# Kernel tuning notes

Hardware: AMD Instinct MI355X
Metric: run time of the kernel (lower is better)

## Reference

```python
import jax, jax.numpy as jnp
import numpy as np

SCALE = 100.0
ACTIVE_EPS = 1e-6


def setup_inputs() -> dict:
    key = jax.random.key(0)
    kq, kk, kv = jax.random.split(key, 3)
    B, K, D = 64, 1024, 512
    return {
        "query": jax.random.normal(kq, (B, D), dtype=jnp.float32),
        "keys": jax.random.normal(kk, (K, D), dtype=jnp.float32),
        "values": jax.random.normal(kv, (K, D), dtype=jnp.float32),
    }


def _scores(query, keys):
    # Fused, batched version of the per-key PureFFN score layers.
    # Layer k has W_up = diag(S * key[k] * d^-0.5) on active dims (|key|>1e-6),
    # b_gate = 1 on active dims, W_down[0] = 1/S on active dims. The extra
    # hidden unit (row `dim`) has zero W_down weight and never contributes.
    # PureFFN: out = W_down @ (h * sigmoid(h + b_gate)), h = W_up @ x.
    D = query.shape[-1]
    scale = D ** -0.5
    active = (jnp.abs(keys) > ACTIVE_EPS).astype(query.dtype)      # [K, D]
    u = (SCALE * scale) * query[:, None, :] * keys[None, :, :]     # [B, K, D]
    g = u * jax.nn.sigmoid(u + active[None, :, :])                 # silu with b_gate=1 on active dims
    return (1.0 / SCALE) * jnp.einsum('bkd,kd->bk', g, active)    # [B, K]


def reference(query, keys, values):
    scores = _scores(query, keys)            # [B, K]
    winner_idx = jnp.argmax(scores, axis=-1)  # [B] int
    out_values = values[winner_idx]           # [B, D] winner-take-all gather
    return out_values, winner_idx
```

## Files before the change

kernel.cpp:

```cpp
#include <hip/hip_runtime.h>
#include <stdint.h>

#define NB 64
#define NK 1024
#define ND 512
#define CHUNKS 16
#define KEYS_PER_BLOCK (NK / CHUNKS)
#define WAVES_PER_BLOCK 4
#define KEYS_PER_WAVE (KEYS_PER_BLOCK / WAVES_PER_BLOCK)

#if __has_builtin(__builtin_amdgcn_exp2f)
#define EXP2F(x) __builtin_amdgcn_exp2f(x)
#else
#define EXP2F(x) exp2f(x)
#endif
#if __has_builtin(__builtin_amdgcn_rcpf)
#define RCPF(x) __builtin_amdgcn_rcpf(x)
#else
#define RCPF(x) (1.0f / (x))
#endif

__device__ __forceinline__ float silu_term(float qc, float kv, float acc) {
    float kz = (fabsf(kv) > 1e-6f) ? kv : 0.0f;
    float u = qc * kz;
    const float NL2E = -1.4426950408889634f;
    float y = fmaf(u, NL2E, NL2E);
    float e = EXP2F(y);
    float r = RCPF(1.0f + e);
    return fmaf(u, r, acc);
}

__device__ __forceinline__ unsigned long long pack_win(float s, int k) {
    uint32_t bits = __float_as_uint(s);
    uint32_t so = (bits & 0x80000000u) ? ~bits : (bits | 0x80000000u);
    return ((unsigned long long)so << 32) | (unsigned long long)(~(uint32_t)k);
}

__global__ __launch_bounds__(256) void sia_scores(const float* __restrict__ q,
                                                  const float* __restrict__ keys,
                                                  unsigned long long* __restrict__ ws) {
    const int bidx = blockIdx.x;
    const int b = bidx >> 4;
    const int chunk = bidx & (CHUNKS - 1);
    const int tid = threadIdx.x;
    const int wave = tid >> 6;
    const int lane = tid & 63;

    const float C = 100.0f * 0.04419417382415922f;

    const float4* q4 = reinterpret_cast<const float4*>(q + b * ND + lane * 8);
    float4 qa = q4[0];
    float4 qb = q4[1];
    qa.x *= C; qa.y *= C; qa.z *= C; qa.w *= C;
    qb.x *= C; qb.y *= C; qb.z *= C; qb.w *= C;

    const int k0 = chunk * KEYS_PER_BLOCK + wave * KEYS_PER_WAVE;

    float acc[KEYS_PER_WAVE];
    #pragma unroll
    for (int i = 0; i < KEYS_PER_WAVE; ++i) {
        const float4* k4 = reinterpret_cast<const float4*>(keys + (k0 + i) * ND + lane * 8);
        float4 ka = k4[0];
        float4 kb = k4[1];
        float p = 0.0f;
        p = silu_term(qa.x, ka.x, p);
        p = silu_term(qa.y, ka.y, p);
        p = silu_term(qa.z, ka.z, p);
        p = silu_term(qa.w, ka.w, p);
        p = silu_term(qb.x, kb.x, p);
        p = silu_term(qb.y, kb.y, p);
        p = silu_term(qb.z, kb.z, p);
        p = silu_term(qb.w, kb.w, p);
        acc[i] = p;
    }

    #pragma unroll
    for (int off = 32; off > 0; off >>= 1) {
        #pragma unroll
        for (int i = 0; i < KEYS_PER_WAVE; ++i)
            acc[i] += __shfl_xor(acc[i], off, 64);
    }

    float best_s = acc[0];
    int best_j = 0;
    #pragma unroll
    for (int i = 1; i < KEYS_PER_WAVE; ++i)
        if (acc[i] > best_s) { best_s = acc[i]; best_j = i; }

    if (lane == 0)
        ws[b * 64 + chunk * WAVES_PER_BLOCK + wave] = pack_win(best_s, k0 + best_j);
}

__global__ __launch_bounds__(64) void sia_final(const unsigned long long* __restrict__ ws,
                                                const float* __restrict__ values,
                                                float* __restrict__ out) {
    const int b = blockIdx.x;
    const int lane = threadIdx.x;

    unsigned long long p = ws[b * 64 + lane];
    #pragma unroll
    for (int off = 32; off > 0; off >>= 1) {
        unsigned long long o = __shfl_xor(p, off, 64);
        if (o > p) p = o;
    }
    const uint32_t k = ~(uint32_t)(p & 0xFFFFFFFFull);

    const float4* v4 = reinterpret_cast<const float4*>(values + (size_t)k * ND) + lane * 2;
    float4* o4 = reinterpret_cast<float4*>(out + b * ND) + lane * 2;
    o4[0] = v4[0];
    o4[1] = v4[1];

    if (lane == 0)
        out[NB * ND + b] = (float)k;
}

extern "C" void kernel_launch(void* const* d_in, const int* in_sizes, int n_in,
                              void* d_out, int out_size, void* d_ws, size_t ws_size,
                              hipStream_t stream) {
    const float* q      = (const float*)d_in[0];
    const float* keys   = (const float*)d_in[1];
    const float* values = (const float*)d_in[2];
    float* out = (float*)d_out;
    unsigned long long* ws = (unsigned long long*)d_ws;

    sia_scores<<<dim3(NB * CHUNKS), dim3(256), 0, stream>>>(q, keys, ws);
    sia_final<<<dim3(NB), dim3(64), 0, stream>>>(ws, values, out);
}
```

Baseline: 19.31 us.

## Process four query rows per block to reuse key loads and hoist masking

Each block now handles four batch rows and a smaller key chunk (64 chunks of 16 keys). Every loaded key vector and its activity mask is reused across the four queries, which cuts global key traffic and repeated mask work. Per-wave winners are reduced in shared memory so each block writes one packed winner per row. The grid size stays the same, but each thread keeps more accumulators and query registers, and the block gains a shared-memory reduction and a __syncthreads.

After: 17.92 us. -7.2%, faster.

```diff
diff --git a/kernel.cpp b/kernel.cpp
--- a/kernel.cpp
+++ b/kernel.cpp
@@ -4,7 +4,8 @@
 #define NB 64
 #define NK 1024
 #define ND 512
-#define CHUNKS 16
+#define ROWS 4
+#define CHUNKS 64
 #define KEYS_PER_BLOCK (NK / CHUNKS)
 #define WAVES_PER_BLOCK 4
 #define KEYS_PER_WAVE (KEYS_PER_BLOCK / WAVES_PER_BLOCK)
@@ -20,8 +21,7 @@
 #define RCPF(x) (1.0f / (x))
 #endif
 
-__device__ __forceinline__ float silu_term(float qc, float kv, float acc) {
-    float kz = (fabsf(kv) > 1e-6f) ? kv : 0.0f;
+__device__ __forceinline__ float silu_acc(float qc, float kz, float acc) {
     float u = qc * kz;
     const float NL2E = -1.4426950408889634f;
     float y = fmaf(u, NL2E, NL2E);
@@ -36,11 +36,15 @@
     return ((unsigned long long)so << 32) | (unsigned long long)(~(uint32_t)k);
 }
 
+__device__ __forceinline__ float msk(float kv) {
+    return (fabsf(kv) > 1e-6f) ? kv : 0.0f;
+}
+
 __global__ __launch_bounds__(256) void sia_scores(const float* __restrict__ q,
                                                   const float* __restrict__ keys,
                                                   unsigned long long* __restrict__ ws) {
     const int bidx = blockIdx.x;
-    const int b = bidx >> 4;
+    const int bg = bidx >> 6;
     const int chunk = bidx & (CHUNKS - 1);
     const int tid = threadIdx.x;
     const int wave = tid >> 6;
@@ -48,47 +52,77 @@
 
     const float C = 100.0f * 0.04419417382415922f;
 
-    const float4* q4 = reinterpret_cast<const float4*>(q + b * ND + lane * 8);
-    float4 qa = q4[0];
-    float4 qb = q4[1];
-    qa.x *= C; qa.y *= C; qa.z *= C; qa.w *= C;
-    qb.x *= C; qb.y *= C; qb.z *= C; qb.w *= C;
+    float4 qa[ROWS], qb[ROWS];
+    #pragma unroll
+    for (int r = 0; r < ROWS; ++r) {
+        const float4* q4 = reinterpret_cast<const float4*>(q + (bg * ROWS + r) * ND + lane * 8);
+        qa[r] = q4[0]; qb[r] = q4[1];
+        qa[r].x *= C; qa[r].y *= C; qa[r].z *= C; qa[r].w *= C;
+        qb[r].x *= C; qb[r].y *= C; qb[r].z *= C; qb[r].w *= C;
+    }
 
     const int k0 = chunk * KEYS_PER_BLOCK + wave * KEYS_PER_WAVE;
 
-    float acc[KEYS_PER_WAVE];
+    float acc[ROWS][KEYS_PER_WAVE];
+    #pragma unroll
+    for (int r = 0; r < ROWS; ++r)
+        #pragma unroll
+        for (int i = 0; i < KEYS_PER_WAVE; ++i)
+            acc[r][i] = 0.0f;
+
     #pragma unroll
     for (int i = 0; i < KEYS_PER_WAVE; ++i) {
         const float4* k4 = reinterpret_cast<const float4*>(keys + (k0 + i) * ND + lane * 8);
         float4 ka = k4[0];
         float4 kb = k4[1];
-        float p = 0.0f;
-        p = silu_term(qa.x, ka.x, p);
-        p = silu_term(qa.y, ka.y, p);
-        p = silu_term(qa.z, ka.z, p);
-        p = silu_term(qa.w, ka.w, p);
-        p = silu_term(qb.x, kb.x, p);
-        p = silu_term(qb.y, kb.y, p);
-        p = silu_term(qb.z, kb.z, p);
-        p = silu_term(qb.w, kb.w, p);
-        acc[i] = p;
+        ka.x = msk(ka.x); ka.y = msk(ka.y); ka.z = msk(ka.z); ka.w = msk(ka.w);
+        kb.x = msk(kb.x); kb.y = msk(kb.y); kb.z = msk(kb.z); kb.w = msk(kb.w);
+        #pragma unroll
+        for (int r = 0; r < ROWS; ++r) {
+            float p = acc[r][i];
+            p = silu_acc(qa[r].x, ka.x, p);
+            p = silu_acc(qa[r].y, ka.y, p);
+            p = silu_acc(qa[r].z, ka.z, p);
+            p = silu_acc(qa[r].w, ka.w, p);
+            p = silu_acc(qb[r].x, kb.x, p);
+            p = silu_acc(qb[r].y, kb.y, p);
+            p = silu_acc(qb[r].z, kb.z, p);
+            p = silu_acc(qb[r].w, kb.w, p);
+            acc[r][i] = p;
+        }
     }
 
     #pragma unroll
     for (int off = 32; off > 0; off >>= 1) {
         #pragma unroll
-        for (int i = 0; i < KEYS_PER_WAVE; ++i)
-            acc[i] += __shfl_xor(acc[i], off, 64);
+        for (int r = 0; r < ROWS; ++r)
+            #pragma unroll
+            for (int i = 0; i < KEYS_PER_WAVE; ++i)
+                acc[r][i] += __shfl_xor(acc[r][i], off, 64);
     }
 
-    float best_s = acc[0];
-    int best_j = 0;
-    #pragma unroll
-    for (int i = 1; i < KEYS_PER_WAVE; ++i)
-        if (acc[i] > best_s) { best_s = acc[i]; best_j = i; }
+    __shared__ unsigned long long win[WAVES_PER_BLOCK][ROWS];
+    if (lane == 0) {
+        #pragma unroll
+        for (int r = 0; r < ROWS; ++r) {
+            float best_s = acc[r][0];
+            int best_j = 0;
+            #pragma unroll
+            for (int i = 1; i < KEYS_PER_WAVE; ++i)
+                if (acc[r][i] > best_s) { best_s = acc[r][i]; best_j = i; }
+            win[wave][r] = pack_win(best_s, k0 + best_j);
+        }
+    }
+    __syncthreads();
 
-    if (lane == 0)
-        ws[b * 64 + chunk * WAVES_PER_BLOCK + wave] = pack_win(best_s, k0 + best_j);
+    if (tid < ROWS) {
+        const int r = tid;
+        unsigned long long p = win[0][r];
+        #pragma unroll
+        for (int w = 1; w < WAVES_PER_BLOCK; ++w)
+            if (win[w][r] > p) p = win[w][r];
+        ws[(bg * ROWS + r) * CHUNKS + chunk] = p;
+    }
 }
 
 __global__ __launch_bounds__(64) void sia_final(const unsigned long long* __restrict__ ws,
@@ -97,7 +131,7 @@
     const int b = blockIdx.x;
     const int lane = threadIdx.x;
 
-    unsigned long long p = ws[b * 64 + lane];
+    unsigned long long p = ws[b * CHUNKS + lane];
     #pragma unroll
     for (int off = 32; off > 0; off >>= 1) {
         unsigned long long o = __shfl_xor(p, off, 64);
@@ -123,6 +157,6 @@
     float* out = (float*)d_out;
     unsigned long long* ws = (unsigned long long*)d_ws;
 
-    sia_scores<<<dim3(NB * CHUNKS), dim3(256), 0, stream>>>(q, keys, ws);
+    sia_scores<<<dim3((NB / ROWS) * CHUNKS), dim3(256), 0, stream>>>(q, keys, ws);
     sia_final<<<dim3(NB), dim3(64), 0, stream>>>(ws, values, out);
 }
```

## Stage masked key chunks in LDS and share them across four query rows

Applied to the files above, without the earlier changes.

Each block now loads a 16-key chunk of keys into shared memory once and applies the activity mask during staging. Four waves then reuse that chunk for four different query rows. Before, each block handled one query row and read its keys straight from global memory. This cuts redundant global and L2 key traffic and removes the per-element mask from the inner loop, at the cost of 32 KB of LDS per block, a barrier, and LDS read bandwidth.

After: 18.52 us. 4.1% less time.

```diff
diff --git a/kernel.cpp b/kernel.cpp
--- a/kernel.cpp
+++ b/kernel.cpp
@@ -4,10 +4,10 @@
 #define NB 64
 #define NK 1024
 #define ND 512
-#define CHUNKS 16
-#define KEYS_PER_BLOCK (NK / CHUNKS)
-#define WAVES_PER_BLOCK 4
-#define KEYS_PER_WAVE (KEYS_PER_BLOCK / WAVES_PER_BLOCK)
+#define CHUNKS 64
+#define KPB (NK / CHUNKS)
+#define RPB 4
+#define RGROUPS (NB / RPB)
 
 #if __has_builtin(__builtin_amdgcn_exp2f)
 #define EXP2F(x) __builtin_amdgcn_exp2f(x)
@@ -20,8 +20,7 @@
 #define RCPF(x) (1.0f / (x))
 #endif
 
-__device__ __forceinline__ float silu_term(float qc, float kv, float acc) {
-    float kz = (fabsf(kv) > 1e-6f) ? kv : 0.0f;
+__device__ __forceinline__ float silu_acc(float qc, float kz, float acc) {
     float u = qc * kz;
     const float NL2E = -1.4426950408889634f;
     float y = fmaf(u, NL2E, NL2E);
@@ -33,14 +32,18 @@
 __device__ __forceinline__ unsigned long long pack_win(float s, int k) {
     uint32_t bits = __float_as_uint(s);
     uint32_t so = (bits & 0x80000000u) ? ~bits : (bits | 0x80000000u);
-    return ((unsigned long long)so << 32) | (unsigned long long)(~(uint32_t)k);
+    return ((unsigned long long)so << 32) | (unsigned long long)(uint32_t)(NK - 1 - k);
+}
+
+__device__ __forceinline__ float msk(float kv) {
+    return (fabsf(kv) > 1e-6f) ? kv : 0.0f;
 }
 
 __global__ __launch_bounds__(256) void sia_scores(const float* __restrict__ q,
                                                   const float* __restrict__ keys,
                                                   unsigned long long* __restrict__ ws) {
     const int bidx = blockIdx.x;
-    const int b = bidx >> 4;
+    const int rg    = bidx >> 6;
     const int chunk = bidx & (CHUNKS - 1);
     const int tid = threadIdx.x;
     const int wave = tid >> 6;
@@ -48,47 +51,59 @@
 
     const float C = 100.0f * 0.04419417382415922f;
 
-    const float4* q4 = reinterpret_cast<const float4*>(q + b * ND + lane * 8);
+    __shared__ float kls[KPB * ND];
+    {
+        const float4* gk = reinterpret_cast<const float4*>(keys + (size_t)chunk * KPB * ND);
+        float4* lk = reinterpret_cast<float4*>(kls);
+        #pragma unroll
+        for (int i = 0; i < (KPB * ND / 4) / 256; ++i) {
+            float4 v = gk[i * 256 + tid];
+            v.x = msk(v.x); v.y = msk(v.y); v.z = msk(v.z); v.w = msk(v.w);
+            lk[i * 256 + tid] = v;
+        }
+    }
+    __syncthreads();
+
+    const int row = rg * RPB + wave;
+    const float4* q4 = reinterpret_cast<const float4*>(q + row * ND + lane * 8);
     float4 qa = q4[0];
     float4 qb = q4[1];
     qa.x *= C; qa.y *= C; qa.z *= C; qa.w *= C;
     qb.x *= C; qb.y *= C; qb.z *= C; qb.w *= C;
 
-    const int k0 = chunk * KEYS_PER_BLOCK + wave * KEYS_PER_WAVE;
-
-    float acc[KEYS_PER_WAVE];
+    float acc[KPB];
     #pragma unroll
-    for (int i = 0; i < KEYS_PER_WAVE; ++i) {
-        const float4* k4 = reinterpret_cast<const float4*>(keys + (k0 + i) * ND + lane * 8);
+    for (int kk = 0; kk < KPB; ++kk) {
+        const float4* k4 = reinterpret_cast<const float4*>(&kls[kk * ND + lane * 8]);
         float4 ka = k4[0];
         float4 kb = k4[1];
         float p = 0.0f;
-        p = silu_term(qa.x, ka.x, p);
-        p = silu_term(qa.y, ka.y, p);
-        p = silu_term(qa.z, ka.z, p);
-        p = silu_term(qa.w, ka.w, p);
-        p = silu_term(qb.x, kb.x, p);
-        p = silu_term(qb.y, kb.y, p);
-        p = silu_term(qb.z, kb.z, p);
-        p = silu_term(qb.w, kb.w, p);
-        acc[i] = p;
+        p = silu_acc(qa.x, ka.x, p);
+        p = silu_acc(qa.y, ka.y, p);
+        p = silu_acc(qa.z, ka.z, p);
+        p = silu_acc(qa.w, ka.w, p);
+        p = silu_acc(qb.x, kb.x, p);
+        p = silu_acc(qb.y, kb.y, p);
+        p = silu_acc(qb.z, kb.z, p);
+        p = silu_acc(qb.w, kb.w, p);
+        acc[kk] = p;
     }
 
     #pragma unroll
     for (int off = 32; off > 0; off >>= 1) {
         #pragma unroll
-        for (int i = 0; i < KEYS_PER_WAVE; ++i)
-            acc[i] += __shfl_xor(acc[i], off, 64);
+        for (int kk = 0; kk < KPB; ++kk)
+            acc[kk] += __shfl_xor(acc[kk], off, 64);
     }
 
-    float best_s = acc[0];
-    int best_j = 0;
-    #pragma unroll
-    for (int i = 1; i < KEYS_PER_WAVE; ++i)
-        if (acc[i] > best_s) { best_s = acc[i]; best_j = i; }
-
-    if (lane == 0)
-        ws[b * 64 + chunk * WAVES_PER_BLOCK + wave] = pack_win(best_s, k0 + best_j);
+    if (lane == 0) {
+        float best_s = acc[0];
+        int best_j = 0;
+        #pragma unroll
+        for (int kk = 1; kk < KPB; ++kk)
+            if (acc[kk] > best_s) { best_s = acc[kk]; best_j = kk; }
+        ws[row * CHUNKS + chunk] = pack_win(best_s, chunk * KPB + best_j);
+    }
 }
 
 __global__ __launch_bounds__(64) void sia_final(const unsigned long long* __restrict__ ws,
@@ -97,13 +112,13 @@
     const int b = blockIdx.x;
     const int lane = threadIdx.x;
 
-    unsigned long long p = ws[b * 64 + lane];
+    unsigned long long p = ws[b * CHUNKS + lane];
     #pragma unroll
     for (int off = 32; off > 0; off >>= 1) {
         unsigned long long o = __shfl_xor(p, off, 64);
         if (o > p) p = o;
     }
-    const uint32_t k = ~(uint32_t)(p & 0xFFFFFFFFull);
+    const int k = NK - 1 - (int)((uint32_t)p & 0x3FFu);
 
     const float4* v4 = reinterpret_cast<const float4*>(values + (size_t)k * ND) + lane * 2;
     float4* o4 = reinterpret_cast<float4*>(out + b * ND) + lane * 2;
@@ -123,6 +138,6 @@
     float* out = (float*)d_out;
     unsigned long long* ws = (unsigned long long*)d_ws;
 
-    sia_scores<<<dim3(NB * CHUNKS), dim3(256), 0, stream>>>(q, keys, ws);
+    sia_scores<<<dim3(RGROUPS * CHUNKS), dim3(256), 0, stream>>>(q, keys, ws);
     sia_final<<<dim3(NB), dim3(64), 0, stream>>>(ws, values, out);
 }
```
